# Kernel optimization log

Measured on AMD Instinct MI355X. Metric: run time of the kernel, lower is better.

## Reference

```python
import jax, jax.numpy as jnp
import numpy as np

N = 100000      # nodes
E = 1600000     # edges (avg degree 16)
F = 128         # feature dim (in == out)
H = 4           # heads
ALPHA = 0.2     # leaky relu slope


def setup_inputs() -> dict:
    key = jax.random.key(0)
    k1, k2, k3, k4, k5 = jax.random.split(key, 5)
    inputs = jax.random.normal(k1, (N, F), dtype=jnp.float32)
    # ensure every node appears as a destination row (src of message) so rowsum > 0
    src = jnp.concatenate([jnp.arange(N, dtype=jnp.int32),
                           jax.random.randint(k2, (E - N,), 0, N, dtype=jnp.int32)])
    dst = jax.random.randint(k3, (E,), 0, N, dtype=jnp.int32)
    edge = jnp.stack([src, dst])  # [2, E], rows = adj.indices()
    adj_values = jax.random.uniform(k4, (E,), dtype=jnp.float32)
    W = jnp.ones((H, F), dtype=jnp.float32)  # nn.init.ones_ per head
    stdv = 1.0 / np.sqrt(2.0 * F)
    a = jax.random.uniform(k5, (H, 2 * F), dtype=jnp.float32, minval=-stdv, maxval=stdv)
    return {"inputs": inputs, "edge": edge, "adj_values": adj_values, "W": W, "a": a}


def reference(inputs, edge, adj_values, W, a):
    src, dst = edge[0], edge[1]
    acc = jnp.zeros_like(inputs)
    for k in range(H):  # small fixed head loop (distinct params per head)
        h = inputs * W[k]                       # [N, F] elementwise scale
        # a.mm([h_src; h_dst]) decomposes into per-node partial scores
        s_src = h @ a[k, :F]                    # [N]
        s_dst = h @ a[k, F:]                    # [N]
        e = jnp.exp(jax.nn.leaky_relu(s_src[src] + s_dst[dst], ALPHA)) * adj_values  # [E]
        rowsum = jax.ops.segment_sum(e, src, num_segments=N)               # [N]
        h_prime = jax.ops.segment_sum(e[:, None] * h[dst], src, num_segments=N)  # [N, F]
        acc = acc + jax.nn.elu(h_prime / rowsum[:, None])  # concat=True -> elu
    return acc / H  # mean over heads
```

## Files before the change

kernel.cpp:

```cpp
#include <hip/hip_runtime.h>

#define FDIM   128
#define HEADS  4
#define ALPHA  0.2f
#define DMASK  0x03FFFFFF
#define PT     4096
#define NBMAX  1568

typedef float v2f __attribute__((ext_vector_type(2)));

__device__ __forceinline__ float readlane_f(float v, int lane) {
  return __int_as_float(__builtin_amdgcn_readlane(__float_as_int(v), lane));
}

__global__ __launch_bounds__(256) void score_kernel(
    const float* __restrict__ x, const float* __restrict__ W,
    const float* __restrict__ a, float* __restrict__ s_src,
    float* __restrict__ s_dst, unsigned int* __restrict__ xb, int n) {
  int lane = threadIdx.x & 63;
  int node = (blockIdx.x << 2) + (threadIdx.x >> 6);
  if (node >= n) return;
  const float2* x2 = (const float2*)x;
  const float2* W2 = (const float2*)W;
  const float2* a2 = (const float2*)a;
  float2 xv = x2[(size_t)node * 64 + lane];

  unsigned int u0 = __float_as_uint(xv.x);
  unsigned int u1 = __float_as_uint(xv.y);
  u0 += 0x7fffu + ((u0 >> 16) & 1u);
  u1 += 0x7fffu + ((u1 >> 16) & 1u);
  xb[(size_t)node * 64 + lane] = (u0 >> 16) | (u1 & 0xffff0000u);

#pragma unroll
  for (int k = 0; k < HEADS; k++) {
    float2 wv = W2[k * 64 + lane];
    float hx = xv.x * wv.x, hy = xv.y * wv.y;
    float2 as_ = a2[k * 128 + lane];
    float2 ad_ = a2[k * 128 + 64 + lane];
    float rs = hx * as_.x + hy * as_.y;
    float rd = hx * ad_.x + hy * ad_.y;
#pragma unroll
    for (int off = 32; off > 0; off >>= 1) {
      rs += __shfl_down(rs, off);
      rd += __shfl_down(rd, off);
    }
    if (lane == 0) {
      s_src[node * HEADS + k] = rs;
      s_dst[node * HEADS + k] = rd;
    }
  }
}

__global__ __launch_bounds__(256) void hist_kernel(const int* __restrict__ src,
                                                   int* __restrict__ hist,
                                                   int E, int NB) {
  __shared__ int h[NBMAX];
  int t = threadIdx.x;
  for (int i = t; i < NB; i += 256) h[i] = 0;
  __syncthreads();
  int base = blockIdx.x * 8192;
#pragma unroll 4
  for (int j = 0; j < 32; j++) {
    int i = base + j * 256 + t;
    if (i < E) atomicAdd(&h[src[i] >> 6], 1);
  }
  __syncthreads();
  for (int i = t; i < NB; i += 256)
    if (h[i]) atomicAdd(&hist[i], h[i]);
}

__global__ __launch_bounds__(256) void scan_kernel(const int* __restrict__ hist,
                                                   int* __restrict__ fine_ptr,
                                                   int* __restrict__ cursor,
                                                   int NB, int E) {
  __shared__ int lds[256];
  int t = threadIdx.x;
  int loc[8];
  int s = 0;
#pragma unroll
  for (int j = 0; j < 8; j++) {
    int idx = t * 8 + j;
    loc[j] = (idx < NB) ? hist[idx] : 0;
    s += loc[j];
  }
  lds[t] = s;
  __syncthreads();
  for (int off = 1; off < 256; off <<= 1) {
    int xv = (t >= off) ? lds[t - off] : 0;
    __syncthreads();
    lds[t] += xv;
    __syncthreads();
  }
  int run = lds[t] - s;
#pragma unroll
  for (int j = 0; j < 8; j++) {
    int idx = t * 8 + j;
    if (idx < NB) {
      fine_ptr[idx] = run;
      cursor[idx]   = run;
    }
    run += loc[j];
  }
  if (t == 0) fine_ptr[NB] = E;
}

__global__ __launch_bounds__(256) void partition_kernel(
    const int* __restrict__ src, const int* __restrict__ dst,
    const float* __restrict__ adj, int* __restrict__ cursor,
    int2* __restrict__ ebuf, int E, int NB) {
  __shared__ int h[NBMAX];
  __shared__ int sc[NBMAX];
  __shared__ int bg[NBMAX];
  __shared__ unsigned short keyarr[PT];
  __shared__ int2 es[PT];
  __shared__ int lds[256];

  int t = threadIdx.x;
  int base = blockIdx.x * PT;
  for (int i = t; i < NB; i += 256) h[i] = 0;
  __syncthreads();

  int ssrc[16];
#pragma unroll
  for (int j = 0; j < 16; j++) {
    int i = base + j * 256 + t;
    ssrc[j] = (i < E) ? src[i] : -1;
    if (ssrc[j] >= 0) atomicAdd(&h[ssrc[j] >> 6], 1);
  }
  __syncthreads();

  int loc[8];
  int s = 0;
#pragma unroll
  for (int j = 0; j < 8; j++) {
    int idx = t * 8 + j;
    loc[j] = (idx < NB) ? h[idx] : 0;
    s += loc[j];
  }
  lds[t] = s;
  __syncthreads();
  for (int off = 1; off < 256; off <<= 1) {
    int xv = (t >= off) ? lds[t - off] : 0;
    __syncthreads();
    lds[t] += xv;
    __syncthreads();
  }
  int run = lds[t] - s;
#pragma unroll
  for (int j = 0; j < 8; j++) {
    int idx = t * 8 + j;
    if (idx < NB) sc[idx] = run;
    run += loc[j];
  }
  __syncthreads();

  for (int i = t; i < NB; i += 256)
    if (h[i]) bg[i] = atomicAdd(&cursor[i], h[i]);
  __syncthreads();

#pragma unroll
  for (int j = 0; j < 16; j++) {
    if (ssrc[j] >= 0) {
      int i = base + j * 256 + t;
      int k = ssrc[j] >> 6;
      int slot = atomicAdd(&sc[k], 1);
      int2 pk;
      pk.x = (int)(((unsigned)(ssrc[j] & 63) << 26) | (unsigned)dst[i]);
      pk.y = __float_as_int(adj[i]);
      es[slot] = pk;
      keyarr[slot] = (unsigned short)k;
    }
  }
  __syncthreads();

  int tc = E - base; if (tc > PT) tc = PT;
  for (int s2 = t; s2 < tc; s2 += 256) {
    int k = keyarr[s2];
    int rank = s2 - (sc[k] - h[k]);
    ebuf[bg[k] + rank] = es[s2];
  }
}

__global__ __launch_bounds__(256, 8) void aggregate_kernel(
    const unsigned int* __restrict__ xb, const float* __restrict__ W,
    const float* __restrict__ s_src, const float* __restrict__ s_dst,
    const int* __restrict__ fine_ptr, const int2* __restrict__ ebuf,
    float* __restrict__ out, int n) {
  __shared__ int2  es[2048];
  __shared__ float evbuf[4][64];
  __shared__ int   nbeg[65];
  __shared__ int   nrun[64];
  __shared__ int   h[64];

  int t = threadIdx.x, b = blockIdx.x;
  int lane = t & 63, wid = t >> 6;
  int beg = fine_ptr[b];
  int L   = fine_ptr[b + 1] - beg;

  if (t < 64) h[t] = 0;
  __syncthreads();
  for (int i = t; i < L; i += 256)
    atomicAdd(&h[(unsigned)ebuf[beg + i].x >> 26], 1);
  __syncthreads();
  if (t < 64) {
    int v = h[t];
#pragma unroll
    for (int off = 1; off < 64; off <<= 1) {
      int u = __shfl_up(v, off);
      if (lane >= off) v += u;
    }
    nbeg[t + 1] = v;
    nrun[t] = v - h[t];
    if (t == 0) nbeg[0] = 0;
  }
  __syncthreads();
  for (int i = t; i < L; i += 256) {
    int2 pk = ebuf[beg + i];
    int kk = (unsigned)pk.x >> 26;
    int slot = atomicAdd(&nrun[kk], 1);
    es[slot] = pk;
  }
  __syncthreads();

  int e = lane >> 2;
  int k = lane & 3;
  const float2* W2 = (const float2*)W;
  float2 wv0 = W2[0 * 64 + lane], wv1 = W2[1 * 64 + lane];
  float2 wv2 = W2[2 * 64 + lane], wv3 = W2[3 * 64 + lane];

  for (int ni = 0; ni < 16; ni++) {
    int nl = wid * 16 + ni;
    int node = (b << 6) + nl;
    if (node >= n) break;
    int eb = nbeg[nl], cnt = nbeg[nl + 1] - eb;
    float ssrc_k = s_src[node * HEADS + k];

    v2f acc0 = {0.f,0.f}, acc1 = {0.f,0.f}, acc2 = {0.f,0.f}, acc3 = {0.f,0.f};
    float rsum = 0.f;

    auto group8 = [&](int dvv, int roff, int slot0) {
      int dd[8];
      unsigned int xw[8];
#pragma unroll
      for (int j = 0; j < 8; j++)
        dd[j] = __builtin_amdgcn_readlane(dvv, (roff + j) * 4);
#pragma unroll
      for (int j = 0; j < 8; j++)
        xw[j] = xb[(unsigned)(dd[j] << 6) + lane];
#pragma unroll
      for (int j = 0; j < 8; j++) {
        const float4 s4 = *(const float4*)&evbuf[wid][(slot0 + j) * 4];
        v2f xv;
        xv.x = __uint_as_float(xw[j] << 16);
        xv.y = __uint_as_float(xw[j] & 0xffff0000u);
        acc0 += s4.x * xv;
        acc1 += s4.y * xv;
        acc2 += s4.z * xv;
        acc3 += s4.w * xv;
      }
    };

    int c = 0;
    while (c < cnt) {
      int cn = cnt - c; if (cn > 16) cn = 16;
      int2 pk{0, 0};
      if (e < cn) pk = es[eb + c + e];
      int dv = pk.x & DMASK;
      float s = ssrc_k + s_dst[dv * HEADS + k];
      s = (s >= 0.f) ? s : ALPHA * s;
      float ev = __expf(s) * __int_as_float(pk.y);
      rsum += ev;
      evbuf[wid][lane] = ev;
      group8(dv, 0, 0);
      if (cn > 8) group8(dv, 8, 8);
      c += 16;
    }

    rsum += __shfl_xor(rsum, 4);
    rsum += __shfl_xor(rsum, 8);
    rsum += __shfl_xor(rsum, 16);
    rsum += __shfl_xor(rsum, 32);
    float r0 = readlane_f(rsum, 0), r1 = readlane_f(rsum, 1);
    float r2 = readlane_f(rsum, 2), r3 = readlane_f(rsum, 3);

    float2 o{0.f, 0.f};
    float hx, hy;
    hx = wv0.x * acc0.x / r0; hy = wv0.y * acc0.y / r0;
    o.x += (hx > 0.f) ? hx : expm1f(hx); o.y += (hy > 0.f) ? hy : expm1f(hy);
    hx = wv1.x * acc1.x / r1; hy = wv1.y * acc1.y / r1;
    o.x += (hx > 0.f) ? hx : expm1f(hx); o.y += (hy > 0.f) ? hy : expm1f(hy);
    hx = wv2.x * acc2.x / r2; hy = wv2.y * acc2.y / r2;
    o.x += (hx > 0.f) ? hx : expm1f(hx); o.y += (hy > 0.f) ? hy : expm1f(hy);
    hx = wv3.x * acc3.x / r3; hy = wv3.y * acc3.y / r3;
    o.x += (hx > 0.f) ? hx : expm1f(hx); o.y += (hy > 0.f) ? hy : expm1f(hy);
    o.x *= 0.25f; o.y *= 0.25f;
    ((float2*)out)[(size_t)node * 64 + lane] = o;
  }
}

extern "C" void kernel_launch(void* const* d_in, const int* in_sizes, int n_in,
                              void* d_out, int out_size, void* d_ws, size_t ws_size,
                              hipStream_t stream) {
  const float* x   = (const float*)d_in[0];
  const int*   edg = (const int*)d_in[1];
  const float* adj = (const float*)d_in[2];
  const float* W   = (const float*)d_in[3];
  const float* a   = (const float*)d_in[4];
  float* out = (float*)d_out;

  int E = in_sizes[2];
  int n = in_sizes[0] / FDIM;
  const int* src = edg;
  const int* dst = edg + E;
  int NB = (n + 63) >> 6;

  auto align = [](size_t v) { return (v + 255) & ~(size_t)255; };
  char* ws = (char*)d_ws;
  int*   fine_ptr = (int*)ws;          ws += align((size_t)(NB + 1) * 4);
  int*   cursor   = (int*)ws;          ws += align((size_t)NB * 4);
  int*   hist     = (int*)ws;          ws += align((size_t)NB * 4);
  int2*  ebuf     = (int2*)ws;         ws += align((size_t)E * 8);
  float* s_src    = (float*)ws;        ws += align((size_t)n * HEADS * 4);
  float* s_dst    = (float*)ws;        ws += align((size_t)n * HEADS * 4);
  unsigned int* xb = (unsigned int*)ws; ws += align((size_t)n * 64 * 4);

  hipMemsetAsync(hist, 0, (size_t)NB * 4, stream);

  score_kernel<<<(n + 3) / 4, 256, 0, stream>>>(x, W, a, s_src, s_dst, xb, n);
  hist_kernel<<<(E + 8191) / 8192, 256, 0, stream>>>(src, hist, E, NB);
  scan_kernel<<<1, 256, 0, stream>>>(hist, fine_ptr, cursor, NB, E);
  partition_kernel<<<(E + PT - 1) / PT, 256, 0, stream>>>(src, dst, adj, cursor,
                                                          ebuf, E, NB);
  aggregate_kernel<<<NB, 256, 0, stream>>>(xb, W, s_src, s_dst, fine_ptr,
                                           ebuf, out, n);
}
```

Baseline: 328.5 us.

## Fuse histogram into score kernel and gather two neighbor rows per wave with 8-byte loads

Merges the edge-source histogram into the score kernel so a separate launch is removed; the first HB blocks also do histogram work. In the aggregate kernel each wave now splits into two halves that each gather a different neighbor row with 8-byte loads, using a shared dvbuf instead of readlane. Partial sums are combined with a cross-half shuffle, and a float4 epilogue is written by 32 lanes. It also lowers the launch-bounds occupancy hint from 8 to 4 to allow more registers, at the cost of fewer resident waves and LDS use by the unused histogram array in every score block.

```diff
diff --git a/kernel.cpp b/kernel.cpp
--- a/kernel.cpp
+++ b/kernel.cpp
@@ -16,57 +16,60 @@
 __global__ __launch_bounds__(256) void score_kernel(
     const float* __restrict__ x, const float* __restrict__ W,
     const float* __restrict__ a, float* __restrict__ s_src,
-    float* __restrict__ s_dst, unsigned int* __restrict__ xb, int n) {
+    float* __restrict__ s_dst, unsigned int* __restrict__ xb,
+    const int* __restrict__ src, int* __restrict__ hist,
+    int E, int HB, int n) {
+  __shared__ int h[NBMAX];
   int lane = threadIdx.x & 63;
   int node = (blockIdx.x << 2) + (threadIdx.x >> 6);
-  if (node >= n) return;
-  const float2* x2 = (const float2*)x;
-  const float2* W2 = (const float2*)W;
-  const float2* a2 = (const float2*)a;
-  float2 xv = x2[(size_t)node * 64 + lane];
-
-  unsigned int u0 = __float_as_uint(xv.x);
-  unsigned int u1 = __float_as_uint(xv.y);
-  u0 += 0x7fffu + ((u0 >> 16) & 1u);
-  u1 += 0x7fffu + ((u1 >> 16) & 1u);
-  xb[(size_t)node * 64 + lane] = (u0 >> 16) | (u1 & 0xffff0000u);
-
-#pragma unroll
-  for (int k = 0; k < HEADS; k++) {
-    float2 wv = W2[k * 64 + lane];
-    float hx = xv.x * wv.x, hy = xv.y * wv.y;
-    float2 as_ = a2[k * 128 + lane];
-    float2 ad_ = a2[k * 128 + 64 + lane];
-    float rs = hx * as_.x + hy * as_.y;
-    float rd = hx * ad_.x + hy * ad_.y;
-#pragma unroll
-    for (int off = 32; off > 0; off >>= 1) {
-      rs += __shfl_down(rs, off);
-      rd += __shfl_down(rd, off);
-    }
-    if (lane == 0) {
-      s_src[node * HEADS + k] = rs;
-      s_dst[node * HEADS + k] = rd;
-    }
-  }
-}
-
-__global__ __launch_bounds__(256) void hist_kernel(const int* __restrict__ src,
-                                                   int* __restrict__ hist,
-                                                   int E, int NB) {
-  __shared__ int h[NBMAX];
-  int t = threadIdx.x;
-  for (int i = t; i < NB; i += 256) h[i] = 0;
-  __syncthreads();
-  int base = blockIdx.x * 8192;
+  if (node < n) {
+    const float2* x2 = (const float2*)x;
+    const float2* W2 = (const float2*)W;
+    const float2* a2 = (const float2*)a;
+    float2 xv = x2[(size_t)node * 64 + lane];
+
+    unsigned int u0 = __float_as_uint(xv.x);
+    unsigned int u1 = __float_as_uint(xv.y);
+    u0 += 0x7fffu + ((u0 >> 16) & 1u);
+    u1 += 0x7fffu + ((u1 >> 16) & 1u);
+    xb[(size_t)node * 64 + lane] = (u0 >> 16) | (u1 & 0xffff0000u);
+
+#pragma unroll
+    for (int k = 0; k < HEADS; k++) {
+      float2 wv = W2[k * 64 + lane];
+      float hx = xv.x * wv.x, hy = xv.y * wv.y;
+      float2 as_ = a2[k * 128 + lane];
+      float2 ad_ = a2[k * 128 + 64 + lane];
+      float rs = hx * as_.x + hy * as_.y;
+      float rd = hx * ad_.x + hy * ad_.y;
+#pragma unroll
+      for (int off = 32; off > 0; off >>= 1) {
+        rs += __shfl_down(rs, off);
+        rd += __shfl_down(rd, off);
+      }
+      if (lane == 0) {
+        s_src[node * HEADS + k] = rs;
+        s_dst[node * HEADS + k] = rd;
+      }
+    }
+  }
+
+  int b = blockIdx.x;
+  if (b < HB) {
+    int t = threadIdx.x;
+    int NB = (n + 63) >> 6;
+    for (int i = t; i < NB; i += 256) h[i] = 0;
+    __syncthreads();
+    int base = b * 8192;
 #pragma unroll 4
-  for (int j = 0; j < 32; j++) {
-    int i = base + j * 256 + t;
-    if (i < E) atomicAdd(&h[src[i] >> 6], 1);
-  }
-  __syncthreads();
-  for (int i = t; i < NB; i += 256)
-    if (h[i]) atomicAdd(&hist[i], h[i]);
+    for (int j = 0; j < 32; j++) {
+      int i = base + j * 256 + t;
+      if (i < E) atomicAdd(&h[src[i] >> 6], 1);
+    }
+    __syncthreads();
+    for (int i = t; i < NB; i += 256)
+      if (h[i]) atomicAdd(&hist[i], h[i]);
+  }
 }
 
 __global__ __launch_bounds__(256) void scan_kernel(const int* __restrict__ hist,
@@ -181,13 +184,14 @@
   }
 }
 
-__global__ __launch_bounds__(256, 8) void aggregate_kernel(
+__global__ __launch_bounds__(256, 4) void aggregate_kernel(
     const unsigned int* __restrict__ xb, const float* __restrict__ W,
     const float* __restrict__ s_src, const float* __restrict__ s_dst,
     const int* __restrict__ fine_ptr, const int2* __restrict__ ebuf,
     float* __restrict__ out, int n) {
   __shared__ int2  es[2048];
   __shared__ float evbuf[4][64];
+  __shared__ int   dvbuf[4][16];
   __shared__ int   nbeg[65];
   __shared__ int   nrun[64];
   __shared__ int   h[64];
@@ -224,9 +228,8 @@
 
   int e = lane >> 2;
   int k = lane & 3;
-  const float2* W2 = (const float2*)W;
-  float2 wv0 = W2[0 * 64 + lane], wv1 = W2[1 * 64 + lane];
-  float2 wv2 = W2[2 * 64 + lane], wv3 = W2[3 * 64 + lane];
+  int half = lane >> 5;
+  int fl = lane & 31;
 
   for (int ni = 0; ni < 16; ni++) {
     int nl = wid * 16 + ni;
@@ -235,29 +238,23 @@
     int eb = nbeg[nl], cnt = nbeg[nl + 1] - eb;
     float ssrc_k = s_src[node * HEADS + k];
 
-    v2f acc0 = {0.f,0.f}, acc1 = {0.f,0.f}, acc2 = {0.f,0.f}, acc3 = {0.f,0.f};
+    v2f aA0{0.f,0.f}, aA1{0.f,0.f}, aA2{0.f,0.f}, aA3{0.f,0.f};
+    v2f aB0{0.f,0.f}, aB1{0.f,0.f}, aB2{0.f,0.f}, aB3{0.f,0.f};
     float rsum = 0.f;
 
-    auto group8 = [&](int dvv, int roff, int slot0) {
-      int dd[8];
-      unsigned int xw[8];
-#pragma unroll
-      for (int j = 0; j < 8; j++)
-        dd[j] = __builtin_amdgcn_readlane(dvv, (roff + j) * 4);
-#pragma unroll
-      for (int j = 0; j < 8; j++)
-        xw[j] = xb[(unsigned)(dd[j] << 6) + lane];
-#pragma unroll
-      for (int j = 0; j < 8; j++) {
-        const float4 s4 = *(const float4*)&evbuf[wid][(slot0 + j) * 4];
-        v2f xv;
-        xv.x = __uint_as_float(xw[j] << 16);
-        xv.y = __uint_as_float(xw[j] & 0xffff0000u);
-        acc0 += s4.x * xv;
-        acc1 += s4.y * xv;
-        acc2 += s4.z * xv;
-        acc3 += s4.w * xv;
-      }
+    auto pair_one = [&](int j) {
+      int dsel = dvbuf[wid][2 * j + half];
+      uint2 xw = *(const uint2*)(xb + ((unsigned)dsel << 6) + (fl << 1));
+      const float4 s4 = *(const float4*)&evbuf[wid][(2 * j + half) * 4];
+      v2f x01, x23;
+      x01.x = __uint_as_float(xw.x << 16);
+      x01.y = __uint_as_float(xw.x & 0xffff0000u);
+      x23.x = __uint_as_float(xw.y << 16);
+      x23.y = __uint_as_float(xw.y & 0xffff0000u);
+      aA0 += s4.x * x01; aB0 += s4.x * x23;
+      aA1 += s4.y * x01; aB1 += s4.y * x23;
+      aA2 += s4.z * x01; aB2 += s4.z * x23;
+      aA3 += s4.w * x01; aB3 += s4.w * x23;
     };
 
     int c = 0;
@@ -271,8 +268,33 @@
       float ev = __expf(s) * __int_as_float(pk.y);
       rsum += ev;
       evbuf[wid][lane] = ev;
-      group8(dv, 0, 0);
-      if (cn > 8) group8(dv, 8, 8);
+      if (k == 0) dvbuf[wid][e] = dv;
+
+      if (cn == 16) {
+        int dsl[8];
+        uint2 xw[8];
+#pragma unroll
+        for (int j = 0; j < 8; j++) dsl[j] = dvbuf[wid][2 * j + half];
+#pragma unroll
+        for (int j = 0; j < 8; j++)
+          xw[j] = *(const uint2*)(xb + ((unsigned)dsl[j] << 6) + (fl << 1));
+#pragma unroll
+        for (int j = 0; j < 8; j++) {
+          const float4 s4 = *(const float4*)&evbuf[wid][(2 * j + half) * 4];
+          v2f x01, x23;
+          x01.x = __uint_as_float(xw[j].x << 16);
+          x01.y = __uint_as_float(xw[j].x & 0xffff0000u);
+          x23.x = __uint_as_float(xw[j].y << 16);
+          x23.y = __uint_as_float(xw[j].y & 0xffff0000u);
+          aA0 += s4.x * x01; aB0 += s4.x * x23;
+          aA1 += s4.y * x01; aB1 += s4.y * x23;
+          aA2 += s4.z * x01; aB2 += s4.z * x23;
+          aA3 += s4.w * x01; aB3 += s4.w * x23;
+        }
+      } else {
+        int npair = (cn + 1) >> 1;
+        for (int j = 0; j < npair; j++) pair_one(j);
+      }
       c += 16;
     }
 
@@ -283,18 +305,36 @@
     float r0 = readlane_f(rsum, 0), r1 = readlane_f(rsum, 1);
     float r2 = readlane_f(rsum, 2), r3 = readlane_f(rsum, 3);
 
-    float2 o{0.f, 0.f};
-    float hx, hy;
-    hx = wv0.x * acc0.x / r0; hy = wv0.y * acc0.y / r0;
-    o.x += (hx > 0.f) ? hx : expm1f(hx); o.y += (hy > 0.f) ? hy : expm1f(hy);
-    hx = wv1.x * acc1.x / r1; hy = wv1.y * acc1.y / r1;
-    o.x += (hx > 0.f) ? hx : expm1f(hx); o.y += (hy > 0.f) ? hy : expm1f(hy);
-    hx = wv2.x * acc2.x / r2; hy = wv2.y * acc2.y / r2;
-    o.x += (hx > 0.f) ? hx : expm1f(hx); o.y += (hy > 0.f) ? hy : expm1f(hy);
-    hx = wv3.x * acc3.x / r3; hy = wv3.y * acc3.y / r3;
-    o.x += (hx > 0.f) ? hx : expm1f(hx); o.y += (hy > 0.f) ? hy : expm1f(hy);
-    o.x *= 0.25f; o.y *= 0.25f;
-    ((float2*)out)[(size_t)node * 64 + lane] = o;
+    aA0.x += __shfl_xor(aA0.x, 32); aA0.y += __shfl_xor(aA0.y, 32);
+    aB0.x += __shfl_xor(aB0.x, 32); aB0.y += __shfl_xor(aB0.y, 32);
+    aA1.x += __shfl_xor(aA1.x, 32); aA1.y += __shfl_xor(aA1.y, 32);
+    aB1.x += __shfl_xor(aB1.x, 32); aB1.y += __shfl_xor(aB1.y, 32);
+    aA2.x += __shfl_xor(aA2.x, 32); aA2.y += __shfl_xor(aA2.y, 32);
+    aB2.x += __shfl_xor(aB2.x, 32); aB2.y += __shfl_xor(aB2.y, 32);
+    aA3.x += __shfl_xor(aA3.x, 32); aA3.y += __shfl_xor(aA3.y, 32);
+    aB3.x += __shfl_xor(aB3.x, 32); aB3.y += __shfl_xor(aB3.y, 32);
+
+    if (lane < 32) {
+      float4 o{0.f, 0.f, 0.f, 0.f};
+      float hx;
+      const float* Wp = W;
+#define EPI(ACCA, ACCB, RR, KK)                                          \
+      {                                                                  \
+        const float4 wv = *(const float4*)&Wp[KK * FDIM + (fl << 2)];    \
+        float inv = 1.0f / RR;                                           \
+        hx = wv.x * ACCA.x * inv; o.x += (hx > 0.f) ? hx : expm1f(hx);   \
+        hx = wv.y * ACCA.y * inv; o.y += (hx > 0.f) ? hx : expm1f(hx);   \
+        hx = wv.z * ACCB.x * inv; o.z += (hx > 0.f) ? hx : expm1f(hx);   \
+        hx = wv.w * ACCB.y * inv; o.w += (hx > 0.f) ? hx : expm1f(hx);   \
+      }
+      EPI(aA0, aB0, r0, 0)
+      EPI(aA1, aB1, r1, 1)
+      EPI(aA2, aB2, r2, 2)
+      EPI(aA3, aB3, r3, 3)
+#undef EPI
+      o.x *= 0.25f; o.y *= 0.25f; o.z *= 0.25f; o.w *= 0.25f;
+      *(float4*)&out[(size_t)node * FDIM + (fl << 2)] = o;
+    }
   }
 }
 
@@ -313,6 +353,7 @@
   const int* src = edg;
   const int* dst = edg + E;
   int NB = (n + 63) >> 6;
+  int HB = (E + 8191) / 8192;
 
   auto align = [](size_t v) { return (v + 255) & ~(size_t)255; };
   char* ws = (char*)d_ws;
@@ -326,8 +367,8 @@
 
   hipMemsetAsync(hist, 0, (size_t)NB * 4, stream);
 
-  score_kernel<<<(n + 3) / 4, 256, 0, stream>>>(x, W, a, s_src, s_dst, xb, n);
-  hist_kernel<<<(E + 8191) / 8192, 256, 0, stream>>>(src, hist, E, NB);
+  score_kernel<<<(n + 3) / 4, 256, 0, stream>>>(x, W, a, s_src, s_dst, xb,
+                                                src, hist, E, HB, n);
   scan_kernel<<<1, 256, 0, stream>>>(hist, fine_ptr, cursor, NB, E);
   partition_kernel<<<(E + PT - 1) / PT, 256, 0, stream>>>(src, dst, adj, cursor,
                                                           ebuf, E, NB);
```

Measured after the change: 333.7 us. Within noise of the previous version (+1.6%).

## Fuse histogram into score kernel and batch 16 gathers per aggregate chunk

Applied to the files above, without the earlier changes.

Merges hist_kernel into score_kernel, so the first HB blocks also build the per-bucket source histogram, which removes one launch. In aggregate_kernel the two 8-edge gather groups become a single unrolled block of 16 readlanes and 16 bf16 row loads. These loads are issued before the exp/score computation to raise memory-level parallelism. The W loads move to the epilogue and launch bounds drop from 8 to 4 waves to allow more registers, at the cost of occupancy and of always loading 16 rows even for short neighbour lists.

```diff
diff --git a/kernel.cpp b/kernel.cpp
--- a/kernel.cpp
+++ b/kernel.cpp
@@ -16,57 +16,60 @@
 __global__ __launch_bounds__(256) void score_kernel(
     const float* __restrict__ x, const float* __restrict__ W,
     const float* __restrict__ a, float* __restrict__ s_src,
-    float* __restrict__ s_dst, unsigned int* __restrict__ xb, int n) {
+    float* __restrict__ s_dst, unsigned int* __restrict__ xb,
+    const int* __restrict__ src, int* __restrict__ hist,
+    int E, int HB, int n) {
+  __shared__ int h[NBMAX];
   int lane = threadIdx.x & 63;
   int node = (blockIdx.x << 2) + (threadIdx.x >> 6);
-  if (node >= n) return;
-  const float2* x2 = (const float2*)x;
-  const float2* W2 = (const float2*)W;
-  const float2* a2 = (const float2*)a;
-  float2 xv = x2[(size_t)node * 64 + lane];
-
-  unsigned int u0 = __float_as_uint(xv.x);
-  unsigned int u1 = __float_as_uint(xv.y);
-  u0 += 0x7fffu + ((u0 >> 16) & 1u);
-  u1 += 0x7fffu + ((u1 >> 16) & 1u);
-  xb[(size_t)node * 64 + lane] = (u0 >> 16) | (u1 & 0xffff0000u);
-
-#pragma unroll
-  for (int k = 0; k < HEADS; k++) {
-    float2 wv = W2[k * 64 + lane];
-    float hx = xv.x * wv.x, hy = xv.y * wv.y;
-    float2 as_ = a2[k * 128 + lane];
-    float2 ad_ = a2[k * 128 + 64 + lane];
-    float rs = hx * as_.x + hy * as_.y;
-    float rd = hx * ad_.x + hy * ad_.y;
-#pragma unroll
-    for (int off = 32; off > 0; off >>= 1) {
-      rs += __shfl_down(rs, off);
-      rd += __shfl_down(rd, off);
-    }
-    if (lane == 0) {
-      s_src[node * HEADS + k] = rs;
-      s_dst[node * HEADS + k] = rd;
-    }
-  }
-}
-
-__global__ __launch_bounds__(256) void hist_kernel(const int* __restrict__ src,
-                                                   int* __restrict__ hist,
-                                                   int E, int NB) {
-  __shared__ int h[NBMAX];
-  int t = threadIdx.x;
-  for (int i = t; i < NB; i += 256) h[i] = 0;
-  __syncthreads();
-  int base = blockIdx.x * 8192;
+  if (node < n) {
+    const float2* x2 = (const float2*)x;
+    const float2* W2 = (const float2*)W;
+    const float2* a2 = (const float2*)a;
+    float2 xv = x2[(size_t)node * 64 + lane];
+
+    unsigned int u0 = __float_as_uint(xv.x);
+    unsigned int u1 = __float_as_uint(xv.y);
+    u0 += 0x7fffu + ((u0 >> 16) & 1u);
+    u1 += 0x7fffu + ((u1 >> 16) & 1u);
+    xb[(size_t)node * 64 + lane] = (u0 >> 16) | (u1 & 0xffff0000u);
+
+#pragma unroll
+    for (int k = 0; k < HEADS; k++) {
+      float2 wv = W2[k * 64 + lane];
+      float hx = xv.x * wv.x, hy = xv.y * wv.y;
+      float2 as_ = a2[k * 128 + lane];
+      float2 ad_ = a2[k * 128 + 64 + lane];
+      float rs = hx * as_.x + hy * as_.y;
+      float rd = hx * ad_.x + hy * ad_.y;
+#pragma unroll
+      for (int off = 32; off > 0; off >>= 1) {
+        rs += __shfl_down(rs, off);
+        rd += __shfl_down(rd, off);
+      }
+      if (lane == 0) {
+        s_src[node * HEADS + k] = rs;
+        s_dst[node * HEADS + k] = rd;
+      }
+    }
+  }
+
+  int b = blockIdx.x;
+  if (b < HB) {
+    int t = threadIdx.x;
+    int NB = (n + 63) >> 6;
+    for (int i = t; i < NB; i += 256) h[i] = 0;
+    __syncthreads();
+    int base = b * 8192;
 #pragma unroll 4
-  for (int j = 0; j < 32; j++) {
-    int i = base + j * 256 + t;
-    if (i < E) atomicAdd(&h[src[i] >> 6], 1);
-  }
-  __syncthreads();
-  for (int i = t; i < NB; i += 256)
-    if (h[i]) atomicAdd(&hist[i], h[i]);
+    for (int j = 0; j < 32; j++) {
+      int i = base + j * 256 + t;
+      if (i < E) atomicAdd(&h[src[i] >> 6], 1);
+    }
+    __syncthreads();
+    for (int i = t; i < NB; i += 256)
+      if (h[i]) atomicAdd(&hist[i], h[i]);
+  }
 }
 
 __global__ __launch_bounds__(256) void scan_kernel(const int* __restrict__ hist,
@@ -181,7 +184,7 @@
   }
 }
 
-__global__ __launch_bounds__(256, 8) void aggregate_kernel(
+__global__ __launch_bounds__(256, 4) void aggregate_kernel(
     const unsigned int* __restrict__ xb, const float* __restrict__ W,
     const float* __restrict__ s_src, const float* __restrict__ s_dst,
     const int* __restrict__ fine_ptr, const int2* __restrict__ ebuf,
@@ -224,9 +227,6 @@
 
   int e = lane >> 2;
   int k = lane & 3;
-  const float2* W2 = (const float2*)W;
-  float2 wv0 = W2[0 * 64 + lane], wv1 = W2[1 * 64 + lane];
-  float2 wv2 = W2[2 * 64 + lane], wv3 = W2[3 * 64 + lane];
 
   for (int ni = 0; ni < 16; ni++) {
     int nl = wid * 16 + ni;
@@ -235,21 +235,35 @@
     int eb = nbeg[nl], cnt = nbeg[nl + 1] - eb;
     float ssrc_k = s_src[node * HEADS + k];
 
-    v2f acc0 = {0.f,0.f}, acc1 = {0.f,0.f}, acc2 = {0.f,0.f}, acc3 = {0.f,0.f};
+    v2f acc0{0.f,0.f}, acc1{0.f,0.f}, acc2{0.f,0.f}, acc3{0.f,0.f};
     float rsum = 0.f;
 
-    auto group8 = [&](int dvv, int roff, int slot0) {
-      int dd[8];
-      unsigned int xw[8];
-#pragma unroll
-      for (int j = 0; j < 8; j++)
-        dd[j] = __builtin_amdgcn_readlane(dvv, (roff + j) * 4);
-#pragma unroll
-      for (int j = 0; j < 8; j++)
-        xw[j] = xb[(unsigned)(dd[j] << 6) + lane];
-#pragma unroll
-      for (int j = 0; j < 8; j++) {
-        const float4 s4 = *(const float4*)&evbuf[wid][(slot0 + j) * 4];
+    int c = 0;
+    while (c < cnt) {
+      int cn = cnt - c; if (cn > 16) cn = 16;
+      int2 pk{0, 0};
+      if (e < cn) pk = es[eb + c + e];
+      int dv = pk.x & DMASK;
+
+      float sdv = s_dst[dv * HEADS + k];
+      int dd[16];
+#pragma unroll
+      for (int j = 0; j < 16; j++)
+        dd[j] = __builtin_amdgcn_readlane(pk.x, j * 4) & DMASK;
+      unsigned int xw[16];
+#pragma unroll
+      for (int j = 0; j < 16; j++)
+        xw[j] = xb[((unsigned)dd[j] << 6) + lane];
+
+      float s = ssrc_k + sdv;
+      s = (s >= 0.f) ? s : ALPHA * s;
+      float ev = __expf(s) * __int_as_float(pk.y);
+      rsum += ev;
+      evbuf[wid][lane] = ev;
+
+#pragma unroll
+      for (int j = 0; j < 16; j++) {
+        const float4 s4 = *(const float4*)&evbuf[wid][j * 4];
         v2f xv;
         xv.x = __uint_as_float(xw[j] << 16);
         xv.y = __uint_as_float(xw[j] & 0xffff0000u);
@@ -258,21 +272,6 @@
         acc2 += s4.z * xv;
         acc3 += s4.w * xv;
       }
-    };
-
-    int c = 0;
-    while (c < cnt) {
-      int cn = cnt - c; if (cn > 16) cn = 16;
-      int2 pk{0, 0};
-      if (e < cn) pk = es[eb + c + e];
-      int dv = pk.x & DMASK;
-      float s = ssrc_k + s_dst[dv * HEADS + k];
-      s = (s >= 0.f) ? s : ALPHA * s;
-      float ev = __expf(s) * __int_as_float(pk.y);
-      rsum += ev;
-      evbuf[wid][lane] = ev;
-      group8(dv, 0, 0);
-      if (cn > 8) group8(dv, 8, 8);
       c += 16;
     }
 
@@ -283,16 +282,29 @@
     float r0 = readlane_f(rsum, 0), r1 = readlane_f(rsum, 1);
     float r2 = readlane_f(rsum, 2), r3 = readlane_f(rsum, 3);
 
+    const float2* W2 = (const float2*)W;
     float2 o{0.f, 0.f};
     float hx, hy;
-    hx = wv0.x * acc0.x / r0; hy = wv0.y * acc0.y / r0;
-    o.x += (hx > 0.f) ? hx : expm1f(hx); o.y += (hy > 0.f) ? hy : expm1f(hy);
-    hx = wv1.x * acc1.x / r1; hy = wv1.y * acc1.y / r1;
-    o.x += (hx > 0.f) ? hx : expm1f(hx); o.y += (hy > 0.f) ? hy : expm1f(hy);
-    hx = wv2.x * acc2.x / r2; hy = wv2.y * acc2.y / r2;
-    o.x += (hx > 0.f) ? hx : expm1f(hx); o.y += (hy > 0.f) ? hy : expm1f(hy);
-    hx = wv3.x * acc3.x / r3; hy = wv3.y * acc3.y / r3;
-    o.x += (hx > 0.f) ? hx : expm1f(hx); o.y += (hy > 0.f) ? hy : expm1f(hy);
+    {
+      float2 wv = W2[0 * 64 + lane];
+      hx = wv.x * acc0.x / r0; hy = wv.y * acc0.y / r0;
+      o.x += (hx > 0.f) ? hx : expm1f(hx); o.y += (hy > 0.f) ? hy : expm1f(hy);
+    }
+    {
+      float2 wv = W2[1 * 64 + lane];
+      hx = wv.x * acc1.x / r1; hy = wv.y * acc1.y / r1;
+      o.x += (hx > 0.f) ? hx : expm1f(hx); o.y += (hy > 0.f) ? hy : expm1f(hy);
+    }
+    {
+      float2 wv = W2[2 * 64 + lane];
+      hx = wv.x * acc2.x / r2; hy = wv.y * acc2.y / r2;
+      o.x += (hx > 0.f) ? hx : expm1f(hx); o.y += (hy > 0.f) ? hy : expm1f(hy);
+    }
+    {
+      float2 wv = W2[3 * 64 + lane];
+      hx = wv.x * acc3.x / r3; hy = wv.y * acc3.y / r3;
+      o.x += (hx > 0.f) ? hx : expm1f(hx); o.y += (hy > 0.f) ? hy : expm1f(hy);
+    }
     o.x *= 0.25f; o.y *= 0.25f;
     ((float2*)out)[(size_t)node * 64 + lane] = o;
   }
@@ -313,6 +325,7 @@
   const int* src = edg;
   const int* dst = edg + E;
   int NB = (n + 63) >> 6;
+  int HB = (E + 8191) / 8192;
 
   auto align = [](size_t v) { return (v + 255) & ~(size_t)255; };
   char* ws = (char*)d_ws;
@@ -326,8 +339,8 @@
 
   hipMemsetAsync(hist, 0, (size_t)NB * 4, stream);
 
-  score_kernel<<<(n + 3) / 4, 256, 0, stream>>>(x, W, a, s_src, s_dst, xb, n);
-  hist_kernel<<<(E + 8191) / 8192, 256, 0, stream>>>(src, hist, E, NB);
+  score_kernel<<<(n + 3) / 4, 256, 0, stream>>>(x, W, a, s_src, s_dst, xb,
+                                                src, hist, E, HB, n);
   scan_kernel<<<1, 256, 0, stream>>>(hist, fine_ptr, cursor, NB, E);
   partition_kernel<<<(E + PT - 1) / PT, 256, 0, stream>>>(src, dst, adj, cursor,
                                                           ebuf, E, NB);
```

New measurement: 320.6 us. 1.02x faster.
